# Optimization experiments

Hardware: AMD Instinct MI355X
Metric: run time of the kernel (lower is better)

## Reference

```python
import jax, jax.numpy as jnp
import numpy as np

NUM_HEADS = 16

def setup_inputs() -> dict:
    key = jax.random.key(0)
    ks = jax.random.split(key, 6)
    B, S, D = 4, 2048, 1024
    sc = 1.0 / np.sqrt(D)
    return {
        "x": jax.random.normal(ks[0], (B, S, D), jnp.float32),
        "Wq": jax.random.normal(ks[1], (D, D), jnp.float32) * sc,
        "Wk": jax.random.normal(ks[2], (D, D), jnp.float32) * sc,
        "Wv": jax.random.normal(ks[3], (D, D), jnp.float32) * sc,
        "Wo": jax.random.normal(ks[4], (D, D), jnp.float32) * sc,
        "bo": jnp.zeros((D,), jnp.float32),
    }

def reference(x, Wq, Wk, Wv, Wo, bo):
    B, S, D = x.shape
    H = NUM_HEADS
    hd = D // H
    # projections (Linear: x @ W^T, but we store W as [d_in, d_out] so x @ W)
    q = (x @ Wq).reshape(B, S, H, hd)
    k = (x @ Wk).reshape(B, S, H, hd)
    v = (x @ Wv).reshape(B, S, H, hd)
    # scores: [B, H, S, S]
    scores = jnp.einsum("bqhd,bkhd->bhqk", q, k) / jnp.sqrt(jnp.asarray(hd, x.dtype))
    attn = jax.nn.softmax(scores, axis=-1)  # dropout p=0.0 (eval) -> identity
    ctx = jnp.einsum("bhqk,bkhd->bqhd", attn, v).reshape(B, S, D)
    return ctx @ Wo + bo
```

## Files before the change

### kernel.cpp

```cpp
#include <hip/hip_runtime.h>
#include <hip/hip_bf16.h>

typedef __bf16 bf16x8 __attribute__((ext_vector_type(8)));
typedef float f32x4 __attribute__((ext_vector_type(4)));

#define D_MODEL 1024
#define SEQ 2048
#define BATCH 4
#define HEADS 16
#define HD 64
#define M_TOT (BATCH * SEQ)
#define QPW 4

static __device__ __forceinline__ unsigned short f2bf(float f) {
  unsigned int u = __float_as_uint(f);
  unsigned int lsb = (u >> 16) & 1u;
  u += 0x7fffu + lsb;
  return (unsigned short)(u >> 16);
}

__global__ __launch_bounds__(256) void cvt_x_kernel(const float* __restrict__ x,
                                                    unsigned short* __restrict__ xb,
                                                    int n4) {
  int i = blockIdx.x * 256 + threadIdx.x;
  if (i >= n4) return;
  const float4 v = reinterpret_cast<const float4*>(x)[i];
  ushort4 o;
  o.x = f2bf(v.x); o.y = f2bf(v.y); o.z = f2bf(v.z); o.w = f2bf(v.w);
  reinterpret_cast<ushort4*>(xb)[i] = o;
}

__global__ __launch_bounds__(256) void transW4_kernel(
    const float* __restrict__ Wq, const float* __restrict__ Wk,
    const float* __restrict__ Wv, const float* __restrict__ Wo,
    unsigned short* __restrict__ WqT, unsigned short* __restrict__ WkT,
    unsigned short* __restrict__ WvT, unsigned short* __restrict__ WoT) {
  const float* W;
  unsigned short* Wt;
  switch (blockIdx.z) {
    case 0: W = Wq; Wt = WqT; break;
    case 1: W = Wk; Wt = WkT; break;
    case 2: W = Wv; Wt = WvT; break;
    default: W = Wo; Wt = WoT; break;
  }
  __shared__ float t[32][33];
  int bx = blockIdx.x * 32;
  int by = blockIdx.y * 32;
  int tx = threadIdx.x, ty = threadIdx.y;
#pragma unroll
  for (int i = 0; i < 32; i += 8)
    t[ty + i][tx] = W[(size_t)(by + ty + i) * D_MODEL + bx + tx];
  __syncthreads();
#pragma unroll
  for (int i = 0; i < 32; i += 8)
    Wt[(size_t)(bx + ty + i) * D_MODEL + by + tx] = f2bf(t[tx][ty + i]);
}

__global__ __launch_bounds__(256) void gemm_qkv_kernel(
    const unsigned short* __restrict__ A, const unsigned short* __restrict__ WqT,
    const unsigned short* __restrict__ WkT, const unsigned short* __restrict__ WvT,
    unsigned short* __restrict__ Qb, unsigned short* __restrict__ Kb,
    unsigned short* __restrict__ Vb, float qscale) {
  __shared__ __align__(16) unsigned short Als[128][72];
  __shared__ __align__(16) unsigned short Bls[128][72];

  const int tid = threadIdx.x;
  const int l = tid & 63;
  const int wave = tid >> 6;
  const int l15 = l & 15;
  const int lk = l >> 4;
  const int wm = wave >> 1, wn = wave & 1;

  const int bid = blockIdx.x;
  const int nid = (bid & 7) * 192 + (bid >> 3);
  const int mblk = nid / 24;
  const int rem = nid % 24;
  const int which = rem >> 3;
  const int nblk = rem & 7;
  const int m0 = mblk << 7, n0 = nblk << 7;

  const unsigned short* Bt = which == 0 ? WqT : (which == 1 ? WkT : WvT);
  const float scale = which == 0 ? qscale : 1.0f;

  f32x4 acc[4][4] = {};

  const int srow = tid >> 3;
  const int scol = (tid & 7) * 8;

  bf16x8 areg[4], breg[4];
#pragma unroll
  for (int i = 0; i < 4; ++i) {
    areg[i] = *reinterpret_cast<const bf16x8*>(&A[(size_t)(m0 + srow + i * 32) * D_MODEL + scol]);
    breg[i] = *reinterpret_cast<const bf16x8*>(&Bt[(size_t)(n0 + srow + i * 32) * D_MODEL + scol]);
  }

  for (int k0 = 0; k0 < D_MODEL; k0 += 64) {
    __syncthreads();
#pragma unroll
    for (int i = 0; i < 4; ++i) {
      *reinterpret_cast<bf16x8*>(&Als[srow + i * 32][scol]) = areg[i];
      *reinterpret_cast<bf16x8*>(&Bls[srow + i * 32][scol]) = breg[i];
    }
    __syncthreads();

    if (k0 + 64 < D_MODEL) {
#pragma unroll
      for (int i = 0; i < 4; ++i) {
        areg[i] = *reinterpret_cast<const bf16x8*>(
            &A[(size_t)(m0 + srow + i * 32) * D_MODEL + k0 + 64 + scol]);
        breg[i] = *reinterpret_cast<const bf16x8*>(
            &Bt[(size_t)(n0 + srow + i * 32) * D_MODEL + k0 + 64 + scol]);
      }
    }

#pragma unroll
    for (int kk = 0; kk < 2; ++kk) {
      bf16x8 af[4], bfr[4];
#pragma unroll
      for (int m = 0; m < 4; ++m)
        af[m] = *reinterpret_cast<const bf16x8*>(&Als[wm * 64 + m * 16 + l15][kk * 32 + lk * 8]);
#pragma unroll
      for (int n = 0; n < 4; ++n)
        bfr[n] = *reinterpret_cast<const bf16x8*>(&Bls[wn * 64 + n * 16 + l15][kk * 32 + lk * 8]);
#pragma unroll
      for (int m = 0; m < 4; ++m)
#pragma unroll
        for (int n = 0; n < 4; ++n)
          acc[m][n] = __builtin_amdgcn_mfma_f32_16x16x32_bf16(af[m], bfr[n], acc[m][n], 0, 0, 0);
    }
  }

  unsigned short* out = which == 0 ? Qb : (which == 1 ? Kb : Vb);
#pragma unroll
  for (int m = 0; m < 4; ++m) {
#pragma unroll
    for (int n = 0; n < 4; ++n) {
      const int row0 = wm * 64 + m * 16 + lk * 4;
      const int col = wn * 64 + n * 16 + l15;
      const int gm0 = m0 + row0;
      const int gn = n0 + col;
      if (which < 2) {
#pragma unroll
        for (int r = 0; r < 4; ++r)
          out[(size_t)(gm0 + r) * D_MODEL + gn] = f2bf(acc[m][n][r] * scale);
      } else {
        int b = gm0 >> 11, s = gm0 & 2047;
        int h = gn >> 6, d = gn & 63;
        size_t base = ((size_t)((b * HEADS + h) * HD + d)) * SEQ + s;
#pragma unroll
        for (int r = 0; r < 4; ++r) out[base + r] = f2bf(acc[m][n][r]);
      }
    }
  }
}

__global__ __launch_bounds__(256) void gemm_out_kernel(
    const unsigned short* __restrict__ A, const unsigned short* __restrict__ Bt,
    float* __restrict__ out, const float* __restrict__ bias) {
  __shared__ __align__(16) unsigned short Als[128][72];
  __shared__ __align__(16) unsigned short Bls[128][72];

  const int tid = threadIdx.x;
  const int l = tid & 63;
  const int wave = tid >> 6;
  const int l15 = l & 15;
  const int lk = l >> 4;
  const int wm = wave >> 1, wn = wave & 1;

  const int nblocks_n = D_MODEL >> 7;
  const int mblk = blockIdx.x / nblocks_n;
  const int nblk = blockIdx.x % nblocks_n;
  const int m0 = mblk << 7, n0 = nblk << 7;

  f32x4 acc[4][4] = {};

  const int srow = tid >> 3;
  const int scol = (tid & 7) * 8;

  bf16x8 areg[4], breg[4];
#pragma unroll
  for (int i = 0; i < 4; ++i) {
    areg[i] = *reinterpret_cast<const bf16x8*>(&A[(size_t)(m0 + srow + i * 32) * D_MODEL + scol]);
    breg[i] = *reinterpret_cast<const bf16x8*>(&Bt[(size_t)(n0 + srow + i * 32) * D_MODEL + scol]);
  }

  for (int k0 = 0; k0 < D_MODEL; k0 += 64) {
    __syncthreads();
#pragma unroll
    for (int i = 0; i < 4; ++i) {
      *reinterpret_cast<bf16x8*>(&Als[srow + i * 32][scol]) = areg[i];
      *reinterpret_cast<bf16x8*>(&Bls[srow + i * 32][scol]) = breg[i];
    }
    __syncthreads();

    if (k0 + 64 < D_MODEL) {
#pragma unroll
      for (int i = 0; i < 4; ++i) {
        areg[i] = *reinterpret_cast<const bf16x8*>(
            &A[(size_t)(m0 + srow + i * 32) * D_MODEL + k0 + 64 + scol]);
        breg[i] = *reinterpret_cast<const bf16x8*>(
            &Bt[(size_t)(n0 + srow + i * 32) * D_MODEL + k0 + 64 + scol]);
      }
    }

#pragma unroll
    for (int kk = 0; kk < 2; ++kk) {
      bf16x8 af[4], bfr[4];
#pragma unroll
      for (int m = 0; m < 4; ++m)
        af[m] = *reinterpret_cast<const bf16x8*>(&Als[wm * 64 + m * 16 + l15][kk * 32 + lk * 8]);
#pragma unroll
      for (int n = 0; n < 4; ++n)
        bfr[n] = *reinterpret_cast<const bf16x8*>(&Bls[wn * 64 + n * 16 + l15][kk * 32 + lk * 8]);
#pragma unroll
      for (int m = 0; m < 4; ++m)
#pragma unroll
        for (int n = 0; n < 4; ++n)
          acc[m][n] = __builtin_amdgcn_mfma_f32_16x16x32_bf16(af[m], bfr[n], acc[m][n], 0, 0, 0);
    }
  }

#pragma unroll
  for (int m = 0; m < 4; ++m) {
#pragma unroll
    for (int n = 0; n < 4; ++n) {
      const int gm0 = m0 + wm * 64 + m * 16 + lk * 4;
      const int gn = n0 + wn * 64 + n * 16 + l15;
      const float bv = bias[gn];
#pragma unroll
      for (int r = 0; r < 4; ++r)
        out[(size_t)(gm0 + r) * D_MODEL + gn] = acc[m][n][r] + bv;
    }
  }
}

__global__ __launch_bounds__(256) void attn_kernel(const unsigned short* __restrict__ Q,
                                                   const unsigned short* __restrict__ Kb,
                                                   const unsigned short* __restrict__ Vt,
                                                   unsigned short* __restrict__ o0,
                                                   unsigned short* __restrict__ o1,
                                                   float* __restrict__ l0,
                                                   float* __restrict__ l1) {
  __shared__ __align__(16) unsigned short Kls[64 * 64];
  __shared__ __align__(16) unsigned short Vls[64 * 64];

  const int tid = threadIdx.x;
  const int l = tid & 63;
  const int wave = tid >> 6;
  const int l15 = l & 15;
  const int lk = l >> 4;

  const int bid = blockIdx.x;
  const int nid = (bid & 7) * 128 + (bid >> 3);
  const int ks = nid & 1;
  const int qt = (nid >> 1) & 7;
  const int bh = nid >> 4;
  const int b = bh >> 4;
  const int h = bh & 15;

  const int qbase = b * SEQ + qt * 256 + wave * 64;
  const int kt0 = ks * 16;

  bf16x8 qf[QPW][2];
#pragma unroll
  for (int qb = 0; qb < QPW; ++qb)
#pragma unroll
    for (int kk = 0; kk < 2; ++kk)
      qf[qb][kk] = *reinterpret_cast<const bf16x8*>(
          &Q[(size_t)(qbase + qb * 16 + l15) * D_MODEL + h * HD + kk * 32 + lk * 8]);

  f32x4 acc[QPW][4] = {};
  float lsum[QPW] = {};

  const int srow = tid >> 2;
  const int sc = tid & 3;
  const int krow = (srow & 32) | ((srow & 4) << 2) | ((srow >> 1) & 12) | (srow & 3);

  const size_t kgbase = ((size_t)b * SEQ) * D_MODEL + h * HD;
  const size_t vgbase = ((size_t)(b * HEADS + h) * HD) * SEQ;

  char* klsb = (char*)Kls;
  char* vlsb = (char*)Vls;

  for (int kt = kt0; kt < kt0 + 16; ++kt) {
    __syncthreads();
    {
#pragma unroll
      for (int i = 0; i < 2; ++i) {
        uint4 kv = *reinterpret_cast<const uint4*>(
            &Kb[kgbase + (size_t)(kt * 64 + srow) * D_MODEL + sc * 8 + i * 32]);
        uint4 vv = *reinterpret_cast<const uint4*>(
            &Vt[vgbase + (size_t)srow * SEQ + kt * 64 + sc * 8 + i * 32]);
        *reinterpret_cast<uint4*>(
            klsb + krow * 128 + ((sc * 16 + i * 64) ^ ((krow & 7) << 4))) = kv;
        *reinterpret_cast<uint4*>(
            vlsb + srow * 128 + ((sc * 16 + i * 64) ^ ((srow & 7) << 4))) = vv;
      }
    }
    __syncthreads();

    f32x4 s[QPW][4] = {};
#pragma unroll
    for (int kk = 0; kk < 2; ++kk) {
      bf16x8 kf[4];
#pragma unroll
      for (int n = 0; n < 4; ++n)
        kf[n] = *reinterpret_cast<const bf16x8*>(
            klsb + (n * 16 + l15) * 128 + ((kk * 64 + lk * 16) ^ ((l15 & 7) << 4)));
#pragma unroll
      for (int qb = 0; qb < QPW; ++qb)
#pragma unroll
        for (int n = 0; n < 4; ++n)
          s[qb][n] = __builtin_amdgcn_mfma_f32_16x16x32_bf16(kf[n], qf[qb][kk], s[qb][n], 0, 0, 0);
    }

    bf16x8 pvv[QPW][2];
#pragma unroll
    for (int qb = 0; qb < QPW; ++qb) {
      float ps = 0.f;
#pragma unroll
      for (int n = 0; n < 4; ++n)
#pragma unroll
        for (int r = 0; r < 4; ++r) {
          float pp = __builtin_amdgcn_exp2f(s[qb][n][r]);
          ps += pp;
          pvv[qb][n >> 1][(n & 1) * 4 + r] = (__bf16)pp;
        }
      lsum[qb] += ps;
    }

#pragma unroll
    for (int kk = 0; kk < 2; ++kk) {
      bf16x8 vf[4];
#pragma unroll
      for (int nd = 0; nd < 4; ++nd)
        vf[nd] = *reinterpret_cast<const bf16x8*>(
            vlsb + (nd * 16 + l15) * 128 + ((kk * 64 + lk * 16) ^ ((l15 & 7) << 4)));
#pragma unroll
      for (int qb = 0; qb < QPW; ++qb)
#pragma unroll
        for (int nd = 0; nd < 4; ++nd)
          acc[qb][nd] = __builtin_amdgcn_mfma_f32_16x16x32_bf16(vf[nd], pvv[qb][kk], acc[qb][nd], 0, 0, 0);
    }
  }

  unsigned short* op = ks ? o1 : o0;
  float* lp = ks ? l1 : l0;
#pragma unroll
  for (int qb = 0; qb < QPW; ++qb) {
    float t = lsum[qb];
    t += __shfl_xor(t, 16);
    t += __shfl_xor(t, 32);
    const float inv = 1.0f / t;
    const int grow = qbase + qb * 16 + l15;
    const size_t row = (size_t)grow * D_MODEL + h * HD;
#pragma unroll
    for (int nd = 0; nd < 4; ++nd) {
      ushort4 ov;
      ov.x = f2bf(acc[qb][nd][0] * inv);
      ov.y = f2bf(acc[qb][nd][1] * inv);
      ov.z = f2bf(acc[qb][nd][2] * inv);
      ov.w = f2bf(acc[qb][nd][3] * inv);
      *reinterpret_cast<ushort4*>(&op[row + nd * 16 + lk * 4]) = ov;
    }
    if (l < 16) lp[grow * HEADS + h] = t;
  }
}

static __device__ __forceinline__ unsigned int comb2(unsigned int u0, unsigned int u1,
                                                     float w0, float w1) {
  float a0 = __uint_as_float((u0 & 0xffffu) << 16);
  float b0 = __uint_as_float(u0 & 0xffff0000u);
  float a1 = __uint_as_float((u1 & 0xffffu) << 16);
  float b1 = __uint_as_float(u1 & 0xffff0000u);
  unsigned int lo = f2bf(a0 * w0 + a1 * w1);
  unsigned int hi = f2bf(b0 * w0 + b1 * w1);
  return lo | (hi << 16);
}

__global__ __launch_bounds__(256) void combine_kernel(unsigned short* __restrict__ o0,
                                                      const unsigned short* __restrict__ o1,
                                                      const float* __restrict__ l0,
                                                      const float* __restrict__ l1) {
  const int i = blockIdx.x * 256 + threadIdx.x;
  const int row = i >> 7;
  const int h = (i & 127) >> 3;
  const float a = l0[row * HEADS + h];
  const float b = l1[row * HEADS + h];
  const float inv = 1.0f / (a + b);
  const float w0 = a * inv, w1 = b * inv;
  const uint4 x0 = reinterpret_cast<const uint4*>(o0)[i];
  const uint4 x1 = reinterpret_cast<const uint4*>(o1)[i];
  uint4 y;
  y.x = comb2(x0.x, x1.x, w0, w1);
  y.y = comb2(x0.y, x1.y, w0, w1);
  y.z = comb2(x0.z, x1.z, w0, w1);
  y.w = comb2(x0.w, x1.w, w0, w1);
  reinterpret_cast<uint4*>(o0)[i] = y;
}

extern "C" void kernel_launch(void* const* d_in, const int* in_sizes, int n_in,
                              void* d_out, int out_size, void* d_ws, size_t ws_size,
                              hipStream_t stream) {
  const float* x = (const float*)d_in[0];
  const float* Wq = (const float*)d_in[1];
  const float* Wk = (const float*)d_in[2];
  const float* Wv = (const float*)d_in[3];
  const float* Wo = (const float*)d_in[4];
  const float* bo = (const float*)d_in[5];

  char* ws = (char*)d_ws;
  const size_t MB = 1u << 20;
  unsigned short* xb = (unsigned short*)(ws + 0 * MB);
  unsigned short* WqT = (unsigned short*)(ws + 16 * MB);
  unsigned short* WkT = (unsigned short*)(ws + 18 * MB);
  unsigned short* WvT = (unsigned short*)(ws + 20 * MB);
  unsigned short* WoT = (unsigned short*)(ws + 22 * MB);
  unsigned short* Qb = (unsigned short*)(ws + 24 * MB);
  unsigned short* Kb = (unsigned short*)(ws + 40 * MB);
  unsigned short* Vt = (unsigned short*)(ws + 56 * MB);
  unsigned short* ctx = (unsigned short*)(ws + 72 * MB);
  float* l0 = (float*)(ws + 16 * MB);
  float* l1 = (float*)(ws + 16 * MB + 512 * 1024);

  int n4 = (M_TOT * D_MODEL) / 4;
  cvt_x_kernel<<<n4 / 256, 256, 0, stream>>>(x, xb, n4);

  transW4_kernel<<<dim3(32, 32, 4), dim3(32, 8), 0, stream>>>(Wq, Wk, Wv, Wo, WqT, WkT, WvT, WoT);

  gemm_qkv_kernel<<<3 * (M_TOT / 128) * (D_MODEL / 128), 256, 0, stream>>>(
      xb, WqT, WkT, WvT, Qb, Kb, Vt, 0.125f * 1.44269504f);

  attn_kernel<<<BATCH * HEADS * (SEQ / 256) * 2, 256, 0, stream>>>(Qb, Kb, Vt, ctx, xb, l0, l1);
  combine_kernel<<<(M_TOT * D_MODEL / 8) / 256, 256, 0, stream>>>(ctx, xb, l0, l1);

  gemm_out_kernel<<<(M_TOT / 128) * (D_MODEL / 128), 256, 0, stream>>>(ctx, WoT, (float*)d_out, bo);
}
```

Before: 200.3 us.

## Rewrite QKV GEMM with 256x256 tiles and direct global-to-LDS double buffering

Replaces the 128x128 QKV projection GEMM with a 512-thread, 256x256-tile kernel. It treats the contiguous WqT/WkT/WvT buffers as one 3072-wide B matrix. Operands are loaded straight into double-buffered, XOR-swizzled LDS with global_load_lds, which removes the register staging and the padded layout. The V-transpose output now uses 4-element vector stores. The aim is more data reuse per tile and less load and sync overhead, at the cost of 128KB of LDS per block, lower occupancy, and only 384 blocks for the whole GPU.

Measured after the change: 203.2 us. No clear change (+1.5%).

```diff
diff --git a/kernel.cpp b/kernel.cpp
--- a/kernel.cpp
+++ b/kernel.cpp
@@ -17,6 +17,12 @@
   unsigned int lsb = (u >> 16) & 1u;
   u += 0x7fffu + lsb;
   return (unsigned short)(u >> 16);
+}
+
+static __device__ __forceinline__ void glds16(const void* g, void* l) {
+  __builtin_amdgcn_global_load_lds(
+      (const __attribute__((address_space(1))) unsigned int*)g,
+      (__attribute__((address_space(3))) unsigned int*)l, 16, 0, 0);
 }
 
 __global__ __launch_bounds__(256) void cvt_x_kernel(const float* __restrict__ x,
@@ -56,99 +62,116 @@
     Wt[(size_t)(bx + ty + i) * D_MODEL + by + tx] = f2bf(t[tx][ty + i]);
 }
 
-__global__ __launch_bounds__(256) void gemm_qkv_kernel(
-    const unsigned short* __restrict__ A, const unsigned short* __restrict__ WqT,
-    const unsigned short* __restrict__ WkT, const unsigned short* __restrict__ WvT,
+__global__ __launch_bounds__(512) void gemm_qkv256_kernel(
+    const unsigned short* __restrict__ A, const unsigned short* __restrict__ Bt,
     unsigned short* __restrict__ Qb, unsigned short* __restrict__ Kb,
     unsigned short* __restrict__ Vb, float qscale) {
-  __shared__ __align__(16) unsigned short Als[128][72];
-  __shared__ __align__(16) unsigned short Bls[128][72];
+  __shared__ __align__(16) unsigned short Als[2][256 * 64];
+  __shared__ __align__(16) unsigned short Bls[2][256 * 64];
 
   const int tid = threadIdx.x;
   const int l = tid & 63;
   const int wave = tid >> 6;
   const int l15 = l & 15;
   const int lk = l >> 4;
-  const int wm = wave >> 1, wn = wave & 1;
+  const int wm = wave >> 2;
+  const int wn = wave & 3;
 
   const int bid = blockIdx.x;
-  const int nid = (bid & 7) * 192 + (bid >> 3);
-  const int mblk = nid / 24;
-  const int rem = nid % 24;
-  const int which = rem >> 3;
-  const int nblk = rem & 7;
-  const int m0 = mblk << 7, n0 = nblk << 7;
-
-  const unsigned short* Bt = which == 0 ? WqT : (which == 1 ? WkT : WvT);
-  const float scale = which == 0 ? qscale : 1.0f;
-
-  f32x4 acc[4][4] = {};
-
-  const int srow = tid >> 3;
-  const int scol = (tid & 7) * 8;
-
-  bf16x8 areg[4], breg[4];
-#pragma unroll
-  for (int i = 0; i < 4; ++i) {
-    areg[i] = *reinterpret_cast<const bf16x8*>(&A[(size_t)(m0 + srow + i * 32) * D_MODEL + scol]);
-    breg[i] = *reinterpret_cast<const bf16x8*>(&Bt[(size_t)(n0 + srow + i * 32) * D_MODEL + scol]);
-  }
-
-  for (int k0 = 0; k0 < D_MODEL; k0 += 64) {
+  const int nid = (bid & 7) * 48 + (bid >> 3);
+  const int mblk = nid / 12, nblk = nid % 12;
+  const int m0 = mblk << 8, n0 = nblk << 8;
+
+  const int sr = tid >> 3;
+  const int scb = ((tid & 7) * 16) ^ ((sr & 7) << 4);
+  const char* Ab = (const char*)A;
+  const char* Bb = (const char*)Bt;
+
+  f32x4 acc[8][4] = {};
+
+#pragma unroll
+  for (int j = 0; j < 4; ++j) {
+    glds16(Ab + (size_t)(m0 + j * 64 + sr) * 2048 + scb,
+           (char*)Als[0] + j * 8192 + tid * 16);
+    glds16(Bb + (size_t)(n0 + j * 64 + sr) * 2048 + scb,
+           (char*)Bls[0] + j * 8192 + tid * 16);
+  }
+  __syncthreads();
+
+  for (int t = 0; t < 16; ++t) {
+    const int cbuf = t & 1;
+    if (t + 1 < 16) {
+      const int nb = cbuf ^ 1;
+      const size_t kb = (size_t)(t + 1) * 128;
+#pragma unroll
+      for (int j = 0; j < 4; ++j) {
+        glds16(Ab + (size_t)(m0 + j * 64 + sr) * 2048 + kb + scb,
+               (char*)Als[nb] + j * 8192 + tid * 16);
+        glds16(Bb + (size_t)(n0 + j * 64 + sr) * 2048 + kb + scb,
+               (char*)Bls[nb] + j * 8192 + tid * 16);
+      }
+    }
+    const char* albs = (const char*)Als[cbuf];
+    const char* blbs = (const char*)Bls[cbuf];
+
+    bf16x8 bf[4][2];
+#pragma unroll
+    for (int ni = 0; ni < 4; ++ni)
+#pragma unroll
+      for (int kk = 0; kk < 2; ++kk) {
+        const int br = wn * 64 + ni * 16 + l15;
+        bf[ni][kk] = *reinterpret_cast<const bf16x8*>(
+            blbs + br * 128 + ((kk * 64 + lk * 16) ^ ((br & 7) << 4)));
+      }
+#pragma unroll
+    for (int q = 0; q < 4; ++q) {
+      bf16x8 af[2][2];
+#pragma unroll
+      for (int d = 0; d < 2; ++d)
+#pragma unroll
+        for (int kk = 0; kk < 2; ++kk) {
+          const int ar = wm * 128 + (q * 2 + d) * 16 + l15;
+          af[d][kk] = *reinterpret_cast<const bf16x8*>(
+              albs + ar * 128 + ((kk * 64 + lk * 16) ^ ((ar & 7) << 4)));
+        }
+#pragma unroll
+      for (int kk = 0; kk < 2; ++kk)
+#pragma unroll
+        for (int d = 0; d < 2; ++d)
+#pragma unroll
+          for (int ni = 0; ni < 4; ++ni)
+            acc[q * 2 + d][ni] = __builtin_amdgcn_mfma_f32_16x16x32_bf16(
+                af[d][kk], bf[ni][kk], acc[q * 2 + d][ni], 0, 0, 0);
+    }
     __syncthreads();
-#pragma unroll
-    for (int i = 0; i < 4; ++i) {
-      *reinterpret_cast<bf16x8*>(&Als[srow + i * 32][scol]) = areg[i];
-      *reinterpret_cast<bf16x8*>(&Bls[srow + i * 32][scol]) = breg[i];
-    }
-    __syncthreads();
-
-    if (k0 + 64 < D_MODEL) {
-#pragma unroll
-      for (int i = 0; i < 4; ++i) {
-        areg[i] = *reinterpret_cast<const bf16x8*>(
-            &A[(size_t)(m0 + srow + i * 32) * D_MODEL + k0 + 64 + scol]);
-        breg[i] = *reinterpret_cast<const bf16x8*>(
-            &Bt[(size_t)(n0 + srow + i * 32) * D_MODEL + k0 + 64 + scol]);
-      }
-    }
-
-#pragma unroll
-    for (int kk = 0; kk < 2; ++kk) {
-      bf16x8 af[4], bfr[4];
-#pragma unroll
-      for (int m = 0; m < 4; ++m)
-        af[m] = *reinterpret_cast<const bf16x8*>(&Als[wm * 64 + m * 16 + l15][kk * 32 + lk * 8]);
-#pragma unroll
-      for (int n = 0; n < 4; ++n)
-        bfr[n] = *reinterpret_cast<const bf16x8*>(&Bls[wn * 64 + n * 16 + l15][kk * 32 + lk * 8]);
-#pragma unroll
-      for (int m = 0; m < 4; ++m)
-#pragma unroll
-        for (int n = 0; n < 4; ++n)
-          acc[m][n] = __builtin_amdgcn_mfma_f32_16x16x32_bf16(af[m], bfr[n], acc[m][n], 0, 0, 0);
-    }
-  }
-
-  unsigned short* out = which == 0 ? Qb : (which == 1 ? Kb : Vb);
-#pragma unroll
-  for (int m = 0; m < 4; ++m) {
-#pragma unroll
-    for (int n = 0; n < 4; ++n) {
-      const int row0 = wm * 64 + m * 16 + lk * 4;
-      const int col = wn * 64 + n * 16 + l15;
-      const int gm0 = m0 + row0;
-      const int gn = n0 + col;
-      if (which < 2) {
+  }
+
+  const int which = n0 >> 10;
+  const int ncol0 = n0 & 1023;
+#pragma unroll
+  for (int mi = 0; mi < 8; ++mi) {
+#pragma unroll
+    for (int ni = 0; ni < 4; ++ni) {
+      const int grow0 = m0 + wm * 128 + mi * 16 + lk * 4;
+      const int wcol = ncol0 + wn * 64 + ni * 16 + l15;
+      if (which == 0) {
 #pragma unroll
         for (int r = 0; r < 4; ++r)
-          out[(size_t)(gm0 + r) * D_MODEL + gn] = f2bf(acc[m][n][r] * scale);
+          Qb[(size_t)(grow0 + r) * D_MODEL + wcol] = f2bf(acc[mi][ni][r] * qscale);
+      } else if (which == 1) {
+#pragma unroll
+        for (int r = 0; r < 4; ++r)
+          Kb[(size_t)(grow0 + r) * D_MODEL + wcol] = f2bf(acc[mi][ni][r]);
       } else {
-        int b = gm0 >> 11, s = gm0 & 2047;
-        int h = gn >> 6, d = gn & 63;
-        size_t base = ((size_t)((b * HEADS + h) * HD + d)) * SEQ + s;
-#pragma unroll
-        for (int r = 0; r < 4; ++r) out[base + r] = f2bf(acc[m][n][r]);
+        const int b = grow0 >> 11, s = grow0 & 2047;
+        const int h = wcol >> 6, d = wcol & 63;
+        ushort4 ov;
+        ov.x = f2bf(acc[mi][ni][0]);
+        ov.y = f2bf(acc[mi][ni][1]);
+        ov.z = f2bf(acc[mi][ni][2]);
+        ov.w = f2bf(acc[mi][ni][3]);
+        *reinterpret_cast<ushort4*>(
+            &Vb[((size_t)((b * HEADS + h) * HD + d)) * SEQ + s]) = ov;
       }
     }
   }
@@ -428,8 +451,7 @@
 
   transW4_kernel<<<dim3(32, 32, 4), dim3(32, 8), 0, stream>>>(Wq, Wk, Wv, Wo, WqT, WkT, WvT, WoT);
 
-  gemm_qkv_kernel<<<3 * (M_TOT / 128) * (D_MODEL / 128), 256, 0, stream>>>(
-      xb, WqT, WkT, WvT, Qb, Kb, Vt, 0.125f * 1.44269504f);
+  gemm_qkv256_kernel<<<384, 512, 0, stream>>>(xb, WqT, Qb, Kb, Vt, 0.125f * 1.44269504f);
 
   attn_kernel<<<BATCH * HEADS * (SEQ / 256) * 2, 256, 0, stream>>>(Qb, Kb, Vt, ctx, xb, l0, l1);
   combine_kernel<<<(M_TOT * D_MODEL / 8) / 256, 256, 0, stream>>>(ctx, xb, l0, l1);
```
